# Optimization experiments

Measured on AMD Instinct MI355X. Metric: run time of the kernel, lower is better.

## Reference

```python
import jax, jax.numpy as jnp
import numpy as np

B, L, C, H = 4, 2048, 1024, 16
D = C // H  # head_dim = 64


def setup_inputs() -> dict:
    key = jax.random.key(0)
    ks = jax.random.split(key, 7)
    x = jax.random.normal(ks[0], (B, L, C), dtype=jnp.float32)
    Wqkv = jax.random.normal(ks[1], (C, 3 * C), dtype=jnp.float32) * 0.02
    bqkv = jnp.zeros((3 * C,), dtype=jnp.float32)
    q_gamma = jnp.ones((H, D), dtype=jnp.float32)
    k_gamma = jnp.ones((H, D), dtype=jnp.float32)
    Wout = jax.random.normal(ks[2], (C, C), dtype=jnp.float32) * 0.02
    bout = jnp.zeros((C,), dtype=jnp.float32)
    return {"x": x, "Wqkv": Wqkv, "bqkv": bqkv, "q_gamma": q_gamma,
            "k_gamma": k_gamma, "Wout": Wout, "bout": bout}


def _mh_rms_norm(t, gamma):
    # F.normalize(x.float(), dim=-1) * gamma * sqrt(dim), cast back to input dtype
    tf = t.astype(jnp.float32)
    n = jnp.sqrt(jnp.sum(tf * tf, axis=-1, keepdims=True))
    normed = tf / jnp.maximum(n, 1e-12)
    return (normed * gamma * jnp.sqrt(jnp.float32(t.shape[-1]))).astype(t.dtype)


def reference(x, Wqkv, bqkv, q_gamma, k_gamma, Wout, bout):
    b, l, c = x.shape
    qkv = (x @ Wqkv + bqkv).reshape(b, l, 3, H, D)
    q, k, v = qkv[:, :, 0], qkv[:, :, 1], qkv[:, :, 2]  # [B, L, H, D]
    q = _mh_rms_norm(q, q_gamma)
    k = _mh_rms_norm(k, k_gamma)
    # scaled dot-product attention in BLHD layout
    scale = 1.0 / jnp.sqrt(jnp.float32(D))
    scores = jnp.einsum('blhd,bmhd->bhlm', q, k) * scale  # [B, H, L, L]
    probs = jax.nn.softmax(scores, axis=-1)
    h = jnp.einsum('bhlm,bmhd->blhd', probs, v)  # [B, L, H, D]
    h = h.reshape(b, l, c)
    return h @ Wout + bout
```

## Files before the change

kernel.cpp:

```cpp
#include <hip/hip_runtime.h>
#include <hip/hip_bf16.h>
#include <cstdint>
#include <cstddef>

#define B_ 4
#define L_ 2048
#define C_ 1024
#define H_ 16
#define D_ 64

typedef __bf16    bf16x2 __attribute__((ext_vector_type(2)));
typedef __bf16    bf16x4 __attribute__((ext_vector_type(4)));
typedef __bf16    bf16x8 __attribute__((ext_vector_type(8)));
typedef _Float16  f16x4  __attribute__((ext_vector_type(4)));
typedef _Float16  f16x8  __attribute__((ext_vector_type(8)));
typedef float     f32x4  __attribute__((ext_vector_type(4)));

typedef const __attribute__((address_space(1))) uint32_t* gas_ptr;
typedef __attribute__((address_space(3))) uint32_t* las_ptr;
__device__ __forceinline__ void gl_lds16(const void* g, void* l) {
    __builtin_amdgcn_global_load_lds((gas_ptr)(uintptr_t)g,
                                     (las_ptr)(uintptr_t)l, 16, 0, 0);
}

__global__ __launch_bounds__(256) void prep_kernel(
    const float* __restrict__ x, _Float16* __restrict__ x16,
    const float* __restrict__ Wqkv, _Float16* __restrict__ Wq16,
    const float* __restrict__ Wout, _Float16* __restrict__ Wo16)
{
    __shared__ float tile[64][65];
    int bid = blockIdx.x;
    const int tid = threadIdx.x;

    if (bid < 8192) {
        int i = (bid * 256 + tid) * 4;
        float4 v = *(const float4*)&x[i];
        f16x4 o = {(_Float16)v.x, (_Float16)v.y, (_Float16)v.z, (_Float16)v.w};
        *(f16x4*)&x16[i] = o;
        return;
    }
    bid -= 8192;
    const float* W; _Float16* Wt; int N, tx, ty;
    if (bid < 768) { W = Wqkv; Wt = Wq16; N = 3072; tx = bid % 48; ty = bid / 48; }
    else { bid -= 768; W = Wout; Wt = Wo16; N = 1024; tx = bid % 16; ty = bid / 16; }
    const int K = 1024;
    const int k0 = ty * 64, n0 = tx * 64;
    for (int i = tid; i < 1024; i += 256) {
        int r = i >> 4, c4 = (i & 15) * 4;
        float4 v = *(const float4*)&W[(size_t)(k0 + r) * N + n0 + c4];
        tile[r][c4 + 0] = v.x; tile[r][c4 + 1] = v.y;
        tile[r][c4 + 2] = v.z; tile[r][c4 + 3] = v.w;
    }
    __syncthreads();
    for (int i = tid; i < 1024; i += 256) {
        int n = i >> 4, k4 = (i & 15) * 4;
        f16x4 o = {(_Float16)tile[k4 + 0][n], (_Float16)tile[k4 + 1][n],
                   (_Float16)tile[k4 + 2][n], (_Float16)tile[k4 + 3][n]};
        *(f16x4*)&Wt[(size_t)(n0 + n) * K + k0 + k4] = o;
    }
}

template <int MODE>
__global__ __launch_bounds__(256) void gemm_f16_bt_kernel(
    const _Float16* __restrict__ A, const _Float16* __restrict__ Bt,
    const float* __restrict__ bias, void* __restrict__ Cout,
    __bf16* __restrict__ vTout, const float* __restrict__ q_gamma,
    const float* __restrict__ k_gamma, int M, int N, int K)
{
    __shared__ __align__(16) char smraw[MODE == 1 ? 34816 : 16384];
    _Float16* Ash = (_Float16*)smraw;
    _Float16* Bsh = Ash + 128 * 32;

    const int tid  = threadIdx.x;
    const int lane = tid & 63;
    const int wv   = tid >> 6;
    const int wm   = wv & 1, wn = wv >> 1;
    const int n16  = lane & 15, quad = lane >> 4;
    const int brow = blockIdx.y * 128;
    const int bcol = blockIdx.x * 128;

    const int srow = lane >> 2;
    const int scol = (lane & 3) * 8;
    const _Float16* gA = A  + (size_t)(brow + wv * 32 + srow) * K + scol;
    const _Float16* gB = Bt + (size_t)(bcol + wv * 32 + srow) * K + scol;
    _Float16* lA0 = &Ash[wv * 1024];
    _Float16* lA1 = &Ash[wv * 1024 + 512];
    _Float16* lB0 = &Bsh[wv * 1024];
    _Float16* lB1 = &Bsh[wv * 1024 + 512];

    f32x4 acc[4][4] = {};

    for (int k0 = 0; k0 < K; k0 += 32) {
        gl_lds16(gA + k0,                  lA0);
        gl_lds16(gA + k0 + 16 * (size_t)K, lA1);
        gl_lds16(gB + k0,                  lB0);
        gl_lds16(gB + k0 + 16 * (size_t)K, lB1);
        __syncthreads();

        f16x8 ar[4], br[4];
        #pragma unroll
        for (int t = 0; t < 4; t++) {
            ar[t] = *(const f16x8*)&Ash[(wm * 64 + t * 16 + n16) * 32 + quad * 8];
            br[t] = *(const f16x8*)&Bsh[(wn * 64 + t * 16 + n16) * 32 + quad * 8];
        }
        #pragma unroll
        for (int i = 0; i < 4; i++)
            #pragma unroll
            for (int j = 0; j < 4; j++)
                acc[i][j] = __builtin_amdgcn_mfma_f32_16x16x32_f16(
                    ar[i], br[j], acc[i][j], 0, 0, 0);
        __syncthreads();
    }

    if (MODE == 0) {
        #pragma unroll
        for (int j = 0; j < 4; j++) {
            const int col = bcol + wn * 64 + j * 16 + n16;
            const float bv = bias[col];
            #pragma unroll
            for (int i = 0; i < 4; i++) {
                const int row0 = brow + wm * 64 + i * 16 + quad * 4;
                #pragma unroll
                for (int r = 0; r < 4; r++)
                    ((float*)Cout)[(size_t)(row0 + r) * N + col] = acc[i][j][r] + bv;
            }
        }
        return;
    }

    const int region = bcol >> 10;
    float bj[4];
    #pragma unroll
    for (int j = 0; j < 4; j++) bj[j] = bias[bcol + wn * 64 + j * 16 + n16];

    if (region < 2) {
        const float* gamma = (region == 0) ? q_gamma : k_gamma;
        const float scl = (region == 0) ? 1.44269504f : 8.0f;
        const int cb = (bcol & 1023) + wn * 64 + n16;
        float gj[4];
        #pragma unroll
        for (int j = 0; j < 4; j++) gj[j] = gamma[cb + j * 16];

        #pragma unroll
        for (int i = 0; i < 4; i++) {
            #pragma unroll
            for (int r = 0; r < 4; r++) {
                float v0 = acc[i][0][r] + bj[0];
                float v1 = acc[i][1][r] + bj[1];
                float v2 = acc[i][2][r] + bj[2];
                float v3 = acc[i][3][r] + bj[3];
                float ss = v0 * v0 + v1 * v1 + v2 * v2 + v3 * v3;
                ss += __shfl_xor(ss, 1, 64);
                ss += __shfl_xor(ss, 2, 64);
                ss += __shfl_xor(ss, 4, 64);
                ss += __shfl_xor(ss, 8, 64);
                const float sc = scl / fmaxf(sqrtf(ss), 1e-12f);
                const int row = brow + wm * 64 + i * 16 + quad * 4 + r;
                __bf16* op = (__bf16*)Cout + (size_t)row * 3072 + bcol + wn * 64 + n16;
                op[ 0] = (__bf16)(v0 * gj[0] * sc);
                op[16] = (__bf16)(v1 * gj[1] * sc);
                op[32] = (__bf16)(v2 * gj[2] * sc);
                op[48] = (__bf16)(v3 * gj[3] * sc);
            }
        }
    } else {
        __syncthreads();
        __bf16* LT = (__bf16*)smraw;
        #pragma unroll
        for (int i = 0; i < 4; i++)
            #pragma unroll
            for (int j = 0; j < 4; j++) {
                const int col = wn * 64 + j * 16 + n16;
                const int row0 = wm * 64 + i * 16 + quad * 4;
                bf16x4 t4 = {(__bf16)(acc[i][j][0] + bj[j]),
                             (__bf16)(acc[i][j][1] + bj[j]),
                             (__bf16)(acc[i][j][2] + bj[j]),
                             (__bf16)(acc[i][j][3] + bj[j])};
                *(bf16x4*)&LT[col * 136 + row0] = t4;
            }
        __syncthreads();
        const int d = tid >> 1, hf = tid & 1;
        const int bidx = brow >> 11;
        const int l0 = (brow & 2047) + hf * 64;
        const int head = ((bcol - 2048) >> 6) + (d >> 6);
        const size_t vb = (((size_t)(bidx * 16 + head)) * 64 + (d & 63)) * 2048 + l0;
        #pragma unroll
        for (int u = 0; u < 8; u++)
            *(bf16x8*)&vTout[vb + u * 8] = *(const bf16x8*)&LT[d * 136 + hf * 64 + u * 8];
    }
}

__global__ __launch_bounds__(256) void attn_mfma_kernel(
    const __bf16* __restrict__ qkv, const __bf16* __restrict__ vT,
    _Float16* __restrict__ h16)
{
    const int tid  = threadIdx.x;
    const int lane = tid & 63;
    const int wv   = tid >> 6;
    const int n16  = lane & 15;
    const int quad = lane >> 4;
    const int qt = blockIdx.x & 15;
    const int hh = (blockIdx.x >> 4) & 15;
    const int bb = blockIdx.x >> 8;
    const int q0 = qt * 128;
    const int w32 = wv * 32;
    const int bh = bb * 16 + hh;

    __shared__ __align__(16) __bf16 smem[(128 + 64 + 64) * 72];
    __bf16* QP  = smem;
    __bf16* Ksm = smem + 128 * 72;
    __bf16* Vtm = smem + 192 * 72;

    #pragma unroll
    for (int t = 0; t < 4; t++) {
        int i = tid + t * 256;
        int r = i >> 3, d8 = (i & 7) * 8;
        *(bf16x8*)&QP[r * 72 + d8] =
            *(const bf16x8*)&qkv[(size_t)(bb * L_ + q0 + r) * 3072 + hh * 64 + d8];
    }
    __syncthreads();

    bf16x8 qf[2][2];
    #pragma unroll
    for (int qg = 0; qg < 2; qg++)
        #pragma unroll
        for (int hf = 0; hf < 2; hf++)
            qf[qg][hf] = *(const bf16x8*)&QP[(w32 + qg * 16 + n16) * 72 + hf * 32 + quad * 8];
    __syncthreads();

    f32x4 O[2][4] = {};
    float l_run[2] = {0.f, 0.f};

    const __bf16* kbase = &qkv[(size_t)(bb * L_) * 3072 + 1024 + hh * 64];
    const __bf16* vbase = &vT[(size_t)bh * 64 * 2048];

    for (int j0 = 0; j0 < L_; j0 += 64) {
        #pragma unroll
        for (int t = 0; t < 2; t++) {
            int i = tid + t * 256;
            int r = i >> 3, d8 = (i & 7) * 8;
            *(bf16x8*)&Ksm[r * 72 + d8] =
                *(const bf16x8*)&kbase[(size_t)(j0 + r) * 3072 + d8];
        }
        #pragma unroll
        for (int t = 0; t < 2; t++) {
            int i = tid + t * 256;
            int d = i >> 3, k8 = (i & 7) * 8;
            *(bf16x8*)&Vtm[d * 72 + k8] =
                *(const bf16x8*)&vbase[(size_t)d * 2048 + j0 + k8];
        }
        __syncthreads();

        f32x4 St[2][4] = {};
        #pragma unroll
        for (int kg = 0; kg < 4; kg++) {
            bf16x8 a0 = *(const bf16x8*)&Ksm[(kg * 16 + n16) * 72 + quad * 8];
            bf16x8 a1 = *(const bf16x8*)&Ksm[(kg * 16 + n16) * 72 + 32 + quad * 8];
            St[0][kg] = __builtin_amdgcn_mfma_f32_16x16x32_bf16(a0, qf[0][0], St[0][kg], 0, 0, 0);
            St[0][kg] = __builtin_amdgcn_mfma_f32_16x16x32_bf16(a1, qf[0][1], St[0][kg], 0, 0, 0);
            St[1][kg] = __builtin_amdgcn_mfma_f32_16x16x32_bf16(a0, qf[1][0], St[1][kg], 0, 0, 0);
            St[1][kg] = __builtin_amdgcn_mfma_f32_16x16x32_bf16(a1, qf[1][1], St[1][kg], 0, 0, 0);
        }

        #pragma unroll
        for (int qg = 0; qg < 2; qg++) {
            const int prow = (w32 + qg * 16 + n16) * 72;
            float ts = 0.f;
            #pragma unroll
            for (int kg = 0; kg < 4; kg++) {
                float p0 = __builtin_amdgcn_exp2f(St[qg][kg][0]);
                float p1 = __builtin_amdgcn_exp2f(St[qg][kg][1]);
                float p2 = __builtin_amdgcn_exp2f(St[qg][kg][2]);
                float p3 = __builtin_amdgcn_exp2f(St[qg][kg][3]);
                bf16x4 t4 = {(__bf16)p0, (__bf16)p1, (__bf16)p2, (__bf16)p3};
                *(bf16x4*)&QP[prow + kg * 16 + quad * 4] = t4;
                ts += (p0 + p1) + (p2 + p3);
            }
            ts += __shfl_xor(ts, 16, 64);
            ts += __shfl_xor(ts, 32, 64);
            l_run[qg] += ts;
        }

        bf16x8 pf[2][2];
        #pragma unroll
        for (int qg = 0; qg < 2; qg++)
            #pragma unroll
            for (int kh = 0; kh < 2; kh++)
                pf[qg][kh] = *(const bf16x8*)&QP[(w32 + qg * 16 + n16) * 72 + kh * 32 + quad * 8];

        #pragma unroll
        for (int dg = 0; dg < 4; dg++) {
            bf16x8 v0 = *(const bf16x8*)&Vtm[(dg * 16 + n16) * 72 + quad * 8];
            bf16x8 v1 = *(const bf16x8*)&Vtm[(dg * 16 + n16) * 72 + 32 + quad * 8];
            O[0][dg] = __builtin_amdgcn_mfma_f32_16x16x32_bf16(v0, pf[0][0], O[0][dg], 0, 0, 0);
            O[0][dg] = __builtin_amdgcn_mfma_f32_16x16x32_bf16(v1, pf[0][1], O[0][dg], 0, 0, 0);
            O[1][dg] = __builtin_amdgcn_mfma_f32_16x16x32_bf16(v0, pf[1][0], O[1][dg], 0, 0, 0);
            O[1][dg] = __builtin_amdgcn_mfma_f32_16x16x32_bf16(v1, pf[1][1], O[1][dg], 0, 0, 0);
        }
        __syncthreads();
    }

    #pragma unroll
    for (int qg = 0; qg < 2; qg++) {
        const float linv = 1.0f / l_run[qg];
        const int q = q0 + w32 + qg * 16 + n16;
        const size_t orow = (size_t)(bb * L_ + q) * 1024 + hh * 64 + quad * 4;
        #pragma unroll
        for (int dg = 0; dg < 4; dg++) {
            f16x4 o = {(_Float16)(O[qg][dg][0] * linv),
                       (_Float16)(O[qg][dg][1] * linv),
                       (_Float16)(O[qg][dg][2] * linv),
                       (_Float16)(O[qg][dg][3] * linv)};
            *(f16x4*)&h16[orow + dg * 16] = o;
        }
    }
}

extern "C" void kernel_launch(void* const* d_in, const int* in_sizes, int n_in,
                              void* d_out, int out_size, void* d_ws, size_t ws_size,
                              hipStream_t stream)
{
    const float* x       = (const float*)d_in[0];
    const float* Wqkv    = (const float*)d_in[1];
    const float* bqkv    = (const float*)d_in[2];
    const float* q_gamma = (const float*)d_in[3];
    const float* k_gamma = (const float*)d_in[4];
    const float* Wout    = (const float*)d_in[5];
    const float* bout    = (const float*)d_in[6];
    float* out = (float*)d_out;

    uint8_t* ws = (uint8_t*)d_ws;
    _Float16* x16   = (_Float16*)(ws);
    _Float16* Wq16  = (_Float16*)(ws + (16ull << 20));
    _Float16* Wo16  = (_Float16*)(ws + (22ull << 20));
    __bf16*   qkv16 = (__bf16*)  (ws + (24ull << 20));
    _Float16* h16   = (_Float16*)(ws + (72ull << 20));
    __bf16*   vT    = (__bf16*)  (ws + (88ull << 20));

    prep_kernel<<<8192 + 768 + 256, 256, 0, stream>>>(x, x16, Wqkv, Wq16, Wout, Wo16);

    gemm_f16_bt_kernel<1><<<dim3(3 * C_ / 128, B_ * L_ / 128), 256, 0, stream>>>(
        x16, Wq16, bqkv, qkv16, vT, q_gamma, k_gamma, B_ * L_, 3 * C_, C_);

    attn_mfma_kernel<<<B_ * H_ * (L_ / 128), 256, 0, stream>>>(qkv16, vT, h16);

    gemm_f16_bt_kernel<0><<<dim3(C_ / 128, B_ * L_ / 128), 256, 0, stream>>>(
        h16, Wo16, bout, out, nullptr, nullptr, nullptr, B_ * L_, C_, C_);
}
```

Baseline: 317.2 us.

## Load K/V tiles via global_load_lds with XOR-swizzled LDS layout and reorder grid

Replaces register-staged K and V tile copies with direct global-to-LDS 16-byte loads. The padded stride-72 layout becomes an unpadded 64-wide layout with an XOR swizzle, so the MFMA fragment reads avoid bank conflicts. The block index mapping now puts the batch-head index in the fastest-varying position, so concurrently running blocks read different heads' K/V, which may change L2 reuse. The aim is to cut VGPR traffic and load-instruction overhead in the attention inner loop. Loads are still not double-buffered, so latency remains exposed behind the barrier.

```diff
diff --git a/kernel.cpp b/kernel.cpp
--- a/kernel.cpp
+++ b/kernel.cpp
@@ -199,17 +199,16 @@
     const int wv   = tid >> 6;
     const int n16  = lane & 15;
     const int quad = lane >> 4;
-    const int qt = blockIdx.x & 15;
-    const int hh = (blockIdx.x >> 4) & 15;
-    const int bb = blockIdx.x >> 8;
+    const int bh = blockIdx.x & 63;
+    const int qt = blockIdx.x >> 6;
+    const int bb = bh >> 4, hh = bh & 15;
     const int q0 = qt * 128;
     const int w32 = wv * 32;
-    const int bh = bb * 16 + hh;
-
-    __shared__ __align__(16) __bf16 smem[(128 + 64 + 64) * 72];
+
+    __shared__ __align__(16) __bf16 smem[128 * 72 + 64 * 64 + 64 * 64];
     __bf16* QP  = smem;
     __bf16* Ksm = smem + 128 * 72;
-    __bf16* Vtm = smem + 192 * 72;
+    __bf16* Vtm = Ksm + 64 * 64;
 
     #pragma unroll
     for (int t = 0; t < 4; t++) {
@@ -228,34 +227,34 @@
             qf[qg][hf] = *(const bf16x8*)&QP[(w32 + qg * 16 + n16) * 72 + hf * 32 + quad * 8];
     __syncthreads();
 
+    const int sr = (wv << 3) + (lane >> 3);
+    const int sc = ((lane & 7) ^ (lane >> 3)) * 8;
+    const __bf16* kp = &qkv[(size_t)(bb * L_ + sr) * 3072 + 1024 + hh * 64 + sc];
+    const __bf16* vp = &vT[((size_t)bh * 64 + sr) * 2048 + sc];
+    __bf16* kl0 = &Ksm[wv * 512];
+    __bf16* kl1 = &Ksm[2048 + wv * 512];
+    __bf16* vl0 = &Vtm[wv * 512];
+    __bf16* vl1 = &Vtm[2048 + wv * 512];
+
+    const int sw0 = ((quad ^ (n16 & 7)) << 3);
+    const int sw1 = (((quad + 4) ^ (n16 & 7)) << 3);
+
     f32x4 O[2][4] = {};
     float l_run[2] = {0.f, 0.f};
 
-    const __bf16* kbase = &qkv[(size_t)(bb * L_) * 3072 + 1024 + hh * 64];
-    const __bf16* vbase = &vT[(size_t)bh * 64 * 2048];
-
     for (int j0 = 0; j0 < L_; j0 += 64) {
-        #pragma unroll
-        for (int t = 0; t < 2; t++) {
-            int i = tid + t * 256;
-            int r = i >> 3, d8 = (i & 7) * 8;
-            *(bf16x8*)&Ksm[r * 72 + d8] =
-                *(const bf16x8*)&kbase[(size_t)(j0 + r) * 3072 + d8];
-        }
-        #pragma unroll
-        for (int t = 0; t < 2; t++) {
-            int i = tid + t * 256;
-            int d = i >> 3, k8 = (i & 7) * 8;
-            *(bf16x8*)&Vtm[d * 72 + k8] =
-                *(const bf16x8*)&vbase[(size_t)d * 2048 + j0 + k8];
-        }
+        gl_lds16(kp + (size_t)j0 * 3072,        kl0);
+        gl_lds16(kp + (size_t)(j0 + 32) * 3072, kl1);
+        gl_lds16(vp + j0,                        vl0);
+        gl_lds16(vp + 32 * 2048 + j0,            vl1);
         __syncthreads();
 
         f32x4 St[2][4] = {};
         #pragma unroll
         for (int kg = 0; kg < 4; kg++) {
-            bf16x8 a0 = *(const bf16x8*)&Ksm[(kg * 16 + n16) * 72 + quad * 8];
-            bf16x8 a1 = *(const bf16x8*)&Ksm[(kg * 16 + n16) * 72 + 32 + quad * 8];
+            const int R = (kg * 16 + n16) * 64;
+            bf16x8 a0 = *(const bf16x8*)&Ksm[R + sw0];
+            bf16x8 a1 = *(const bf16x8*)&Ksm[R + sw1];
             St[0][kg] = __builtin_amdgcn_mfma_f32_16x16x32_bf16(a0, qf[0][0], St[0][kg], 0, 0, 0);
             St[0][kg] = __builtin_amdgcn_mfma_f32_16x16x32_bf16(a1, qf[0][1], St[0][kg], 0, 0, 0);
             St[1][kg] = __builtin_amdgcn_mfma_f32_16x16x32_bf16(a0, qf[1][0], St[1][kg], 0, 0, 0);
@@ -290,8 +289,9 @@
 
         #pragma unroll
         for (int dg = 0; dg < 4; dg++) {
-            bf16x8 v0 = *(const bf16x8*)&Vtm[(dg * 16 + n16) * 72 + quad * 8];
-            bf16x8 v1 = *(const bf16x8*)&Vtm[(dg * 16 + n16) * 72 + 32 + quad * 8];
+            const int R = (dg * 16 + n16) * 64;
+            bf16x8 v0 = *(const bf16x8*)&Vtm[R + sw0];
+            bf16x8 v1 = *(const bf16x8*)&Vtm[R + sw1];
             O[0][dg] = __builtin_amdgcn_mfma_f32_16x16x32_bf16(v0, pf[0][0], O[0][dg], 0, 0, 0);
             O[0][dg] = __builtin_amdgcn_mfma_f32_16x16x32_bf16(v1, pf[0][1], O[0][dg], 0, 0, 0);
             O[1][dg] = __builtin_amdgcn_mfma_f32_16x16x32_bf16(v0, pf[1][0], O[1][dg], 0, 0, 0);
```

After: 324.4 us. 1.02x slower.
